# Kernel optimization log

Hardware: AMD Instinct MI355X
Metric: run time of the kernel (lower is better)

Reference implementation:

```python
import jax, jax.numpy as jnp
import numpy as np

N = 20000          # num_node
E = 160000         # num edges (avg degree 8)
IN_N = 64          # in_features_node
IN_E = 32          # in_features_edge
HN = 64            # nhid_node
HE = 64            # nhid_edge
KAPPA = 0.9
ITERS = 8          # fixed Picard iterations for the equilibrium solve


def setup_inputs() -> dict:
    key = jax.random.key(0)
    ks = jax.random.split(key, 16)
    f32 = jnp.float32

    def w(k, shape, fan_in):
        return (jax.random.normal(k, shape, dtype=f32) / np.sqrt(fan_in)).astype(f32)

    return {
        # graph structure (int constants)
        "R": jax.random.randint(ks[0], (E,), 0, N),   # receiver node per edge
        "S": jax.random.randint(ks[1], (E,), 0, N),   # sender node per edge
        "H": jax.random.randint(ks[2], (E,), 0, N),   # edge->node aggregation index
        # features (features-first layout, as in the torch code)
        "node_data": jax.random.normal(ks[3], (IN_N, N), dtype=f32),
        "Ra_data": jax.random.normal(ks[4], (IN_E, E), dtype=f32),
        # INECN_Layer parameters
        "W_es": w(ks[5], (HE, HN), HN),      # sender-message weight
        "W_er": w(ks[6], (HE, HN), HN),      # receiver-message weight
        "Omega_e": w(ks[7], (HE, IN_E), IN_E),
        "Wn": w(ks[8], (HN, HN), HN),        # implicit node-state weight
        "Bm": w(ks[9], (HN, HE), HE),        # edge->node mixing
        "Omega_n": w(ks[10], (HN, IN_N), IN_N),
        # dense head (V_0: nhid->nhid, V_1: nhid->in_features_node)
        "V0_w": w(ks[11], (HN, HN), HN),
        "V0_b": jnp.zeros((HN,), dtype=f32),
        "V1_w": w(ks[12], (IN_N, HN), HN),
        "V1_b": jnp.zeros((IN_N,), dtype=f32),
    }


def reference(R, S, H, node_data, Ra_data, W_es, W_er, Omega_e, Wn, Bm,
              Omega_n, V0_w, V0_b, V1_w, V1_b):
    # spectral-norm style contraction: ||kappa * Wn / ||Wn|||| <= kappa (adj_rho = 1)
    Wn_hat = (KAPPA * Wn) / jnp.maximum(jnp.linalg.norm(Wn), 1.0)

    bias_e = Omega_e @ Ra_data        # [HE, E] injected edge features
    bias_n = Omega_n @ node_data      # [HN, N] injected node features

    def step(X, _):
        # edge update: messages from sender/receiver node states
        He_logits = W_es @ X[:, S] + W_er @ X[:, R] + bias_e      # [HE, E]
        He = jax.nn.relu(He_logits)
        # aggregate edge states back to nodes
        agg = jax.ops.segment_sum(He.T, H, num_segments=N).T      # [HE, N] -> [HE, N]
        # implicit node update (contraction => convergent fixed point)
        X_new = jax.nn.relu(Wn_hat @ X + Bm @ agg + bias_n)       # [HN, N]
        return X_new, None

    X0 = jnp.zeros((HN, N), dtype=node_data.dtype)
    X, _ = jax.lax.scan(step, X0, None, length=ITERS)

    # final edge states / logits at the (approximate) fixed point
    He_logits3 = W_es @ X[:, S] + W_er @ X[:, R] + bias_e         # [HE, E]
    He = jax.nn.relu(He_logits3)

    # dense head: x = V_1(dropout(relu(V_0(x.T))))  (eval mode: dropout = identity)
    x = X.T                                                        # [N, HN]
    x = jax.nn.relu(x @ V0_w.T + V0_b)                             # [N, HN]
    x = x @ V1_w.T + V1_b                                          # [N, IN_N]
    return (x, He, He_logits3)
```

## Files before the change

### kernel.cpp

```cpp
#include <hip/hip_runtime.h>
#include <math.h>

#define KAPPA 0.9f
#define ST 68
#define TN 32

typedef unsigned short u16;

__device__ __forceinline__ float relu_f(float v) { return fmaxf(v, 0.0f); }
__device__ __forceinline__ float bf_lo(unsigned u) { return __uint_as_float(u << 16); }
__device__ __forceinline__ float bf_hi(unsigned u) { return __uint_as_float(u & 0xFFFF0000u); }
__device__ __forceinline__ u16 f2bf(float x) {
  unsigned u = __float_as_uint(x);
  return (u16)((u + 0x7FFFu + ((u >> 16) & 1u)) >> 16);
}
__device__ __forceinline__ unsigned pack2(float a, float b) {
  return (unsigned)f2bf(a) | ((unsigned)f2bf(b) << 16);
}

__global__ __launch_bounds__(256) void wnhat_kernel(const float* __restrict__ Wn,
                                                    float* __restrict__ Wn_hat) {
  __shared__ float red[4];
  int t = threadIdx.x;
  float v[16];
  float s = 0.f;
#pragma unroll
  for (int j = 0; j < 16; ++j) { v[j] = Wn[t + 256 * j]; s += v[j] * v[j]; }
#pragma unroll
  for (int off = 32; off > 0; off >>= 1) s += __shfl_down(s, off, 64);
  if ((t & 63) == 0) red[t >> 6] = s;
  __syncthreads();
  float norm = sqrtf(red[0] + red[1] + red[2] + red[3]);
  float scale = KAPPA / fmaxf(norm, 1.0f);
#pragma unroll
  for (int j = 0; j < 16; ++j) Wn_hat[t + 256 * j] = v[j] * scale;
}

__global__ __launch_bounds__(256) void bias_n_kernel(const float* __restrict__ node_data,
                                                     const float* __restrict__ Om_n,
                                                     float* __restrict__ bias_n, int N) {
  __shared__ float NdT[64][ST];
  __shared__ float Om[64][ST];
  int t = threadIdx.x;
  int n_base = blockIdx.x * 64;
#pragma unroll
  for (int j = 0; j < 16; ++j) {
    int f = t + 256 * j;
    int r = f >> 6, c = f & 63;
    float val = (n_base + c < N) ? node_data[(size_t)r * N + n_base + c] : 0.f;
    NdT[c][r] = val;
    Om[r][c] = Om_n[f];
  }
  __syncthreads();
  int ni = t & 15, h4 = (t >> 4) * 4;
  float acc[4][4] = {};
#pragma unroll 4
  for (int k = 0; k < 64; k += 4) {
    float4 a[4], w[4];
#pragma unroll
    for (int i = 0; i < 4; ++i) a[i] = *(const float4*)&NdT[ni + 16 * i][k];
#pragma unroll
    for (int j = 0; j < 4; ++j) w[j] = *(const float4*)&Om[h4 + j][k];
#pragma unroll
    for (int i = 0; i < 4; ++i)
#pragma unroll
      for (int j = 0; j < 4; ++j)
        acc[i][j] += a[i].x * w[j].x + a[i].y * w[j].y + a[i].z * w[j].z + a[i].w * w[j].w;
  }
#pragma unroll
  for (int i = 0; i < 4; ++i) {
    int n = n_base + ni + 16 * i;
    if (n < N) {
      float4 o = make_float4(acc[i][0], acc[i][1], acc[i][2], acc[i][3]);
      *(float4*)&bias_n[(size_t)n * 64 + h4] = o;
    }
  }
}

__global__ void hist_kernel(const int* __restrict__ H, int* __restrict__ count, int E) {
  int e = blockIdx.x * 256 + threadIdx.x;
  if (e < E) atomicAdd(&count[H[e]], 1);
}

__global__ __launch_bounds__(256) void scan_kernel(int* count, int* row_off, int* cursor,
                                                   int N, int E) {
  __shared__ int offs[256];
  __shared__ int sums[256];
  int t = threadIdx.x;
  int chunk = (N + 255) / 256;
  int lo = t * chunk, hi = min(lo + chunk, N);
  int s = 0;
  for (int n = lo; n < hi; ++n) s += count[n];
  sums[t] = s;
  __syncthreads();
  if (t == 0) {
    int run = 0;
    for (int i = 0; i < 256; ++i) { offs[i] = run; run += sums[i]; }
  }
  __syncthreads();
  int run = offs[t];
  for (int n = lo; n < hi; ++n) {
    int c = count[n];
    row_off[n] = run;
    cursor[n] = run;
    run += c;
  }
  if (t == 0) row_off[N] = E;
}

__global__ void scatter_kernel(const int* __restrict__ H, const int* __restrict__ S,
                               const int* __restrict__ R, int* cursor,
                               int2* __restrict__ SRs, int* __restrict__ inv_perm, int E) {
  int e = blockIdx.x * 256 + threadIdx.x;
  if (e < E) {
    int h = H[e];
    int pos = atomicAdd(&cursor[h], 1);
    SRs[pos] = make_int2(S[e], R[e]);
    inv_perm[e] = pos;
  }
}

__global__ __launch_bounds__(256) void bias_build_kernel(const float* __restrict__ Ra,
                                                         const float* __restrict__ Om_e,
                                                         const int* __restrict__ inv_perm,
                                                         u16* __restrict__ bias_sb, int E) {
  __shared__ float OmT[64][36];
  __shared__ float RaT[64][36];
  int t = threadIdx.x;
  int e_base = blockIdx.x * 64;
#pragma unroll
  for (int j = 0; j < 8; ++j) {
    int f = t + 256 * j;
    int r = f >> 5, c = f & 31;
    OmT[r][c] = Om_e[f];
  }
#pragma unroll
  for (int j = 0; j < 8; ++j) {
    int f = t + 256 * j;
    int r = f >> 6, c = f & 63;
    int ee = e_base + c;
    RaT[c][r] = (ee < E) ? Ra[(size_t)r * E + ee] : 0.f;
  }
  __syncthreads();
  int ei = t & 15, h4 = (t >> 4) * 4;
  float acc[4][4] = {};
#pragma unroll 4
  for (int jj = 0; jj < 32; jj += 4) {
    float4 ra[4], om[4];
#pragma unroll
    for (int i = 0; i < 4; ++i) ra[i] = *(const float4*)&RaT[ei + 16 * i][jj];
#pragma unroll
    for (int j = 0; j < 4; ++j) om[j] = *(const float4*)&OmT[h4 + j][jj];
#pragma unroll
    for (int i = 0; i < 4; ++i)
#pragma unroll
      for (int j = 0; j < 4; ++j)
        acc[i][j] += ra[i].x * om[j].x + ra[i].y * om[j].y + ra[i].z * om[j].z +
                     ra[i].w * om[j].w;
  }
#pragma unroll
  for (int i = 0; i < 4; ++i) {
    int e = e_base + ei + 16 * i;
    if (e < E) {
      int p = inv_perm[e];
      uint2 o;
      o.x = pack2(acc[i][0], acc[i][1]);
      o.y = pack2(acc[i][2], acc[i][3]);
      *(uint2*)&bias_sb[((size_t)p << 6) + h4] = o;
    }
  }
}

template <int FIRST>
__global__ __launch_bounds__(256) void agg_kernel(
    const u16* __restrict__ MSb_in, const u16* __restrict__ MRb_in,
    const u16* __restrict__ bias_sb, const int2* __restrict__ SRs,
    const int* __restrict__ row_off, float* __restrict__ agg, int N) {
  __shared__ float part[4][8][ST];
  int t = threadIdx.x;
  int nl = t >> 5, sp = (t >> 3) & 3, q8 = t & 7;
  int nd = blockIdx.x * 8 + nl;
  float a[8] = {};
  if (nd < N) {
    int r0 = row_off[nd], r1 = row_off[nd + 1];
    for (int p = r0 + sp; p < r1; p += 8) {
      int p1 = p + 4;
      bool has1 = p1 < r1;
      int pc1 = has1 ? p1 : p;
      uint4 bv0 = *(const uint4*)&bias_sb[((size_t)p << 6) + q8 * 8];
      uint4 bv1 = *(const uint4*)&bias_sb[((size_t)pc1 << 6) + q8 * 8];
      if (FIRST) {
        a[0] += relu_f(bf_lo(bv0.x)); a[1] += relu_f(bf_hi(bv0.x));
        a[2] += relu_f(bf_lo(bv0.y)); a[3] += relu_f(bf_hi(bv0.y));
        a[4] += relu_f(bf_lo(bv0.z)); a[5] += relu_f(bf_hi(bv0.z));
        a[6] += relu_f(bf_lo(bv0.w)); a[7] += relu_f(bf_hi(bv0.w));
        if (has1) {
          a[0] += relu_f(bf_lo(bv1.x)); a[1] += relu_f(bf_hi(bv1.x));
          a[2] += relu_f(bf_lo(bv1.y)); a[3] += relu_f(bf_hi(bv1.y));
          a[4] += relu_f(bf_lo(bv1.z)); a[5] += relu_f(bf_hi(bv1.z));
          a[6] += relu_f(bf_lo(bv1.w)); a[7] += relu_f(bf_hi(bv1.w));
        }
      } else {
        int2 sr0 = SRs[p];
        int2 sr1 = SRs[pc1];
        uint4 mv0 = *(const uint4*)&MSb_in[((size_t)sr0.x << 6) + q8 * 8];
        uint4 rv0 = *(const uint4*)&MRb_in[((size_t)sr0.y << 6) + q8 * 8];
        uint4 mv1 = *(const uint4*)&MSb_in[((size_t)sr1.x << 6) + q8 * 8];
        uint4 rv1 = *(const uint4*)&MRb_in[((size_t)sr1.y << 6) + q8 * 8];
        a[0] += relu_f(bf_lo(mv0.x) + bf_lo(rv0.x) + bf_lo(bv0.x));
        a[1] += relu_f(bf_hi(mv0.x) + bf_hi(rv0.x) + bf_hi(bv0.x));
        a[2] += relu_f(bf_lo(mv0.y) + bf_lo(rv0.y) + bf_lo(bv0.y));
        a[3] += relu_f(bf_hi(mv0.y) + bf_hi(rv0.y) + bf_hi(bv0.y));
        a[4] += relu_f(bf_lo(mv0.z) + bf_lo(rv0.z) + bf_lo(bv0.z));
        a[5] += relu_f(bf_hi(mv0.z) + bf_hi(rv0.z) + bf_hi(bv0.z));
        a[6] += relu_f(bf_lo(mv0.w) + bf_lo(rv0.w) + bf_lo(bv0.w));
        a[7] += relu_f(bf_hi(mv0.w) + bf_hi(rv0.w) + bf_hi(bv0.w));
        if (has1) {
          a[0] += relu_f(bf_lo(mv1.x) + bf_lo(rv1.x) + bf_lo(bv1.x));
          a[1] += relu_f(bf_hi(mv1.x) + bf_hi(rv1.x) + bf_hi(bv1.x));
          a[2] += relu_f(bf_lo(mv1.y) + bf_lo(rv1.y) + bf_lo(bv1.y));
          a[3] += relu_f(bf_hi(mv1.y) + bf_hi(rv1.y) + bf_hi(bv1.y));
          a[4] += relu_f(bf_lo(mv1.z) + bf_lo(rv1.z) + bf_lo(bv1.z));
          a[5] += relu_f(bf_hi(mv1.z) + bf_hi(rv1.z) + bf_hi(bv1.z));
          a[6] += relu_f(bf_lo(mv1.w) + bf_lo(rv1.w) + bf_lo(bv1.w));
          a[7] += relu_f(bf_hi(mv1.w) + bf_hi(rv1.w) + bf_hi(bv1.w));
        }
      }
    }
  }
  *(float4*)&part[sp][nl][q8 * 8] = make_float4(a[0], a[1], a[2], a[3]);
  *(float4*)&part[sp][nl][q8 * 8 + 4] = make_float4(a[4], a[5], a[6], a[7]);
  __syncthreads();
  if (sp == 0 && nd < N) {
#pragma unroll
    for (int u = 0; u < 2; ++u) {
      float4 s0 = *(const float4*)&part[0][nl][q8 * 8 + 4 * u];
      float4 s1 = *(const float4*)&part[1][nl][q8 * 8 + 4 * u];
      float4 s2 = *(const float4*)&part[2][nl][q8 * 8 + 4 * u];
      float4 s3 = *(const float4*)&part[3][nl][q8 * 8 + 4 * u];
      float4 o = make_float4(s0.x + s1.x + s2.x + s3.x, s0.y + s1.y + s2.y + s3.y,
                             s0.z + s1.z + s2.z + s3.z, s0.w + s1.w + s2.w + s3.w);
      *(float4*)&agg[(size_t)nd * 64 + q8 * 8 + 4 * u] = o;
    }
  }
}

template <int FIRST, int LAST>
__global__ __launch_bounds__(256) void node_kernel(
    const float* __restrict__ X, const float* __restrict__ agg,
    const float* __restrict__ bias_n, const float* __restrict__ Wn_hat,
    const float* __restrict__ Bm, const float* __restrict__ W_es,
    const float* __restrict__ W_er, const float* __restrict__ V0_w,
    const float* __restrict__ V0_b, const float* __restrict__ V1_w,
    const float* __restrict__ V1_b, float* __restrict__ Xout,
    u16* __restrict__ MSb_out, u16* __restrict__ MRb_out,
    float* __restrict__ head_out, int N) {
  __shared__ float Wa[64][ST], Wb[64][ST];
  __shared__ float Xsh[TN][ST], Ash[TN][ST];
  __shared__ float b0s[64], b1s[64];
  int t = threadIdx.x;
  int n_base = blockIdx.x * TN;
#pragma unroll
  for (int j = 0; j < 16; ++j) {
    int f = t + 256 * j;
    int r = f >> 6, c = f & 63;
    Wa[r][c] = Wn_hat[f];
    Wb[r][c] = Bm[f];
  }
  int n8 = t >> 3;
  int q8 = t & 7;
  int nd = n_base + n8;
  bool ok = nd < N;
  if (!FIRST) {
    float4 x0 = make_float4(0, 0, 0, 0), x1 = x0;
    if (ok) {
      x0 = *(const float4*)&X[(size_t)nd * 64 + q8 * 8];
      x1 = *(const float4*)&X[(size_t)nd * 64 + q8 * 8 + 4];
    }
    *(float4*)&Xsh[n8][q8 * 8] = x0;
    *(float4*)&Xsh[n8][q8 * 8 + 4] = x1;
  }
  {
    float4 a0 = make_float4(0, 0, 0, 0), a1 = a0;
    if (ok) {
      a0 = *(const float4*)&agg[(size_t)nd * 64 + q8 * 8];
      a1 = *(const float4*)&agg[(size_t)nd * 64 + q8 * 8 + 4];
    }
    *(float4*)&Ash[n8][q8 * 8] = a0;
    *(float4*)&Ash[n8][q8 * 8 + 4] = a1;
  }
  __syncthreads();
  int ni = t & 15, h4 = (t >> 4) * 4;
  float acc[2][4] = {};
#pragma unroll 4
  for (int k = 0; k < 64; k += 4) {
    float4 xv[2], av[2], wv[4], bv[4];
#pragma unroll
    for (int i = 0; i < 2; ++i) {
      if (!FIRST) xv[i] = *(const float4*)&Xsh[ni + 16 * i][k];
      av[i] = *(const float4*)&Ash[ni + 16 * i][k];
    }
#pragma unroll
    for (int j = 0; j < 4; ++j) {
      wv[j] = *(const float4*)&Wa[h4 + j][k];
      bv[j] = *(const float4*)&Wb[h4 + j][k];
    }
#pragma unroll
    for (int i = 0; i < 2; ++i)
#pragma unroll
      for (int j = 0; j < 4; ++j) {
        float v = av[i].x * bv[j].x + av[i].y * bv[j].y + av[i].z * bv[j].z +
                  av[i].w * bv[j].w;
        if (!FIRST)
          v += xv[i].x * wv[j].x + xv[i].y * wv[j].y + xv[i].z * wv[j].z +
               xv[i].w * wv[j].w;
        acc[i][j] += v;
      }
  }
  __syncthreads();
#pragma unroll
  for (int i = 0; i < 2; ++i) {
    int nn = n_base + ni + 16 * i;
    float4 bb = make_float4(0, 0, 0, 0);
    if (nn < N) bb = *(const float4*)&bias_n[(size_t)nn * 64 + h4];
    float x0 = relu_f(acc[i][0] + bb.x);
    float x1 = relu_f(acc[i][1] + bb.y);
    float x2 = relu_f(acc[i][2] + bb.z);
    float x3 = relu_f(acc[i][3] + bb.w);
    if (!LAST && nn < N)
      *(float4*)&Xout[(size_t)nn * 64 + h4] = make_float4(x0, x1, x2, x3);
    *(float4*)&Xsh[ni + 16 * i][h4] = make_float4(x0, x1, x2, x3);
  }
#pragma unroll
  for (int j = 0; j < 16; ++j) {
    int f = t + 256 * j;
    int r = f >> 6, c = f & 63;
    Wa[r][c] = W_es[f];
    Wb[r][c] = W_er[f];
  }
  __syncthreads();
  {
    float ma[2][4] = {}, ra[2][4] = {};
#pragma unroll 4
    for (int k = 0; k < 64; k += 4) {
      float4 xv[2], ws[4], wr[4];
#pragma unroll
      for (int i = 0; i < 2; ++i) xv[i] = *(const float4*)&Xsh[ni + 16 * i][k];
#pragma unroll
      for (int j = 0; j < 4; ++j) {
        ws[j] = *(const float4*)&Wa[h4 + j][k];
        wr[j] = *(const float4*)&Wb[h4 + j][k];
      }
#pragma unroll
      for (int i = 0; i < 2; ++i)
#pragma unroll
        for (int j = 0; j < 4; ++j) {
          ma[i][j] += xv[i].x * ws[j].x + xv[i].y * ws[j].y + xv[i].z * ws[j].z +
                      xv[i].w * ws[j].w;
          ra[i][j] += xv[i].x * wr[j].x + xv[i].y * wr[j].y + xv[i].z * wr[j].z +
                      xv[i].w * wr[j].w;
        }
    }
#pragma unroll
    for (int i = 0; i < 2; ++i) {
      int nn = n_base + ni + 16 * i;
      if (nn < N) {
        uint2 om, orr;
        om.x = pack2(ma[i][0], ma[i][1]);
        om.y = pack2(ma[i][2], ma[i][3]);
        orr.x = pack2(ra[i][0], ra[i][1]);
        orr.y = pack2(ra[i][2], ra[i][3]);
        *(uint2*)&MSb_out[((size_t)nn << 6) + h4] = om;
        *(uint2*)&MRb_out[((size_t)nn << 6) + h4] = orr;
      }
    }
  }
  if (LAST) {
    __syncthreads();
#pragma unroll
    for (int j = 0; j < 16; ++j) {
      int f = t + 256 * j;
      int r = f >> 6, c = f & 63;
      Wa[r][c] = V0_w[f];
      Wb[r][c] = V1_w[f];
    }
    if (t < 64) b0s[t] = V0_b[t];
    else if (t < 128) b1s[t - 64] = V1_b[t - 64];
    __syncthreads();
    float c1[2][4] = {};
#pragma unroll 4
    for (int k = 0; k < 64; k += 4) {
      float4 xv[2], wv[4];
#pragma unroll
      for (int i = 0; i < 2; ++i) xv[i] = *(const float4*)&Xsh[ni + 16 * i][k];
#pragma unroll
      for (int j = 0; j < 4; ++j) wv[j] = *(const float4*)&Wa[h4 + j][k];
#pragma unroll
      for (int i = 0; i < 2; ++i)
#pragma unroll
        for (int j = 0; j < 4; ++j)
          c1[i][j] += xv[i].x * wv[j].x + xv[i].y * wv[j].y + xv[i].z * wv[j].z +
                      xv[i].w * wv[j].w;
    }
    __syncthreads();
#pragma unroll
    for (int i = 0; i < 2; ++i) {
      float4 o;
      o.x = relu_f(c1[i][0] + b0s[h4 + 0]);
      o.y = relu_f(c1[i][1] + b0s[h4 + 1]);
      o.z = relu_f(c1[i][2] + b0s[h4 + 2]);
      o.w = relu_f(c1[i][3] + b0s[h4 + 3]);
      *(float4*)&Xsh[ni + 16 * i][h4] = o;
    }
    __syncthreads();
    float c2[2][4] = {};
#pragma unroll 4
    for (int k = 0; k < 64; k += 4) {
      float4 xv[2], wv[4];
#pragma unroll
      for (int i = 0; i < 2; ++i) xv[i] = *(const float4*)&Xsh[ni + 16 * i][k];
#pragma unroll
      for (int j = 0; j < 4; ++j) wv[j] = *(const float4*)&Wb[h4 + j][k];
#pragma unroll
      for (int i = 0; i < 2; ++i)
#pragma unroll
        for (int j = 0; j < 4; ++j)
          c2[i][j] += xv[i].x * wv[j].x + xv[i].y * wv[j].y + xv[i].z * wv[j].z +
                      xv[i].w * wv[j].w;
    }
#pragma unroll
    for (int i = 0; i < 2; ++i) {
      int nn = n_base + ni + 16 * i;
      if (nn < N) {
        float4 o;
        o.x = c2[i][0] + b1s[h4 + 0];
        o.y = c2[i][1] + b1s[h4 + 1];
        o.z = c2[i][2] + b1s[h4 + 2];
        o.w = c2[i][3] + b1s[h4 + 3];
        *(float4*)&head_out[(size_t)nn * 64 + h4] = o;
      }
    }
  }
}

__global__ __launch_bounds__(256) void edge_final_kernel(
    const u16* __restrict__ MSb, const u16* __restrict__ MRb,
    const int* __restrict__ S, const int* __restrict__ R,
    const float* __restrict__ Om_e, const float* __restrict__ Ra,
    float* __restrict__ He_out, float* __restrict__ Hel_out, int E) {
  __shared__ float T[64][ST];
  __shared__ float pool2[4608];
  int t = threadIdx.x;
  int e_base = blockIdx.x * 64;
#pragma unroll
  for (int j = 0; j < 8; ++j) {
    int f = t + 256 * j;
    int r = f >> 5, c = f & 31;
    pool2[r * 36 + c] = Om_e[f];
  }
#pragma unroll
  for (int j = 0; j < 8; ++j) {
    int f = t + 256 * j;
    int r = f >> 6, c = f & 63;
    int e2 = e_base + c;
    pool2[2304 + c * 36 + r] = (e2 < E) ? Ra[(size_t)r * E + e2] : 0.f;
  }
  {
    int e = t >> 2, q = t & 3;
    int ee = e_base + e;
    int ec = (ee < E) ? ee : 0;
    int s = S[ec], r = R[ec];
    const u16* mp = &MSb[((size_t)s << 6) + q * 16];
    const u16* rp = &MRb[((size_t)r << 6) + q * 16];
    uint4 m0 = *(const uint4*)mp;
    uint4 m1 = *(const uint4*)(mp + 8);
    uint4 r0 = *(const uint4*)rp;
    uint4 r1 = *(const uint4*)(rp + 8);
    float* tp = &T[e][q * 16];
    tp[0] = bf_lo(m0.x) + bf_lo(r0.x);
    tp[1] = bf_hi(m0.x) + bf_hi(r0.x);
    tp[2] = bf_lo(m0.y) + bf_lo(r0.y);
    tp[3] = bf_hi(m0.y) + bf_hi(r0.y);
    tp[4] = bf_lo(m0.z) + bf_lo(r0.z);
    tp[5] = bf_hi(m0.z) + bf_hi(r0.z);
    tp[6] = bf_lo(m0.w) + bf_lo(r0.w);
    tp[7] = bf_hi(m0.w) + bf_hi(r0.w);
    tp[8] = bf_lo(m1.x) + bf_lo(r1.x);
    tp[9] = bf_hi(m1.x) + bf_hi(r1.x);
    tp[10] = bf_lo(m1.y) + bf_lo(r1.y);
    tp[11] = bf_hi(m1.y) + bf_hi(r1.y);
    tp[12] = bf_lo(m1.z) + bf_lo(r1.z);
    tp[13] = bf_hi(m1.z) + bf_hi(r1.z);
    tp[14] = bf_lo(m1.w) + bf_lo(r1.w);
    tp[15] = bf_hi(m1.w) + bf_hi(r1.w);
  }
  __syncthreads();
  int ei = t & 15, h4 = (t >> 4) * 4;
  float acc[4][4] = {};
#pragma unroll 4
  for (int jj = 0; jj < 32; jj += 4) {
    float4 ra[4], om[4];
#pragma unroll
    for (int i = 0; i < 4; ++i)
      ra[i] = *(const float4*)&pool2[2304 + (ei + 16 * i) * 36 + jj];
#pragma unroll
    for (int j = 0; j < 4; ++j) om[j] = *(const float4*)&pool2[(h4 + j) * 36 + jj];
#pragma unroll
    for (int i = 0; i < 4; ++i)
#pragma unroll
      for (int j = 0; j < 4; ++j)
        acc[i][j] += ra[i].x * om[j].x + ra[i].y * om[j].y + ra[i].z * om[j].z +
                     ra[i].w * om[j].w;
  }
#pragma unroll
  for (int i = 0; i < 4; ++i) {
    float4 tv = *(const float4*)&T[ei + 16 * i][h4];
    acc[i][0] += tv.x;
    acc[i][1] += tv.y;
    acc[i][2] += tv.z;
    acc[i][3] += tv.w;
  }
  __syncthreads();
#pragma unroll
  for (int i = 0; i < 4; ++i)
#pragma unroll
    for (int j = 0; j < 4; ++j)
      pool2[(ei + 16 * i) * 65 + h4 + j] = acc[i][j];
  __syncthreads();
  {
    int e4 = (t & 15) * 4, h0 = t >> 4;
#pragma unroll
    for (int rep = 0; rep < 4; ++rep) {
      int h = h0 + 16 * rep;
      float4 v;
      v.x = pool2[(e4 + 0) * 65 + h];
      v.y = pool2[(e4 + 1) * 65 + h];
      v.z = pool2[(e4 + 2) * 65 + h];
      v.w = pool2[(e4 + 3) * 65 + h];
      size_t idx = (size_t)h * E + e_base + e4;
      if (e_base + e4 < E) {
        *(float4*)&Hel_out[idx] = v;
        float4 u = make_float4(relu_f(v.x), relu_f(v.y), relu_f(v.z), relu_f(v.w));
        *(float4*)&He_out[idx] = u;
      }
    }
  }
}

extern "C" void kernel_launch(void* const* d_in, const int* in_sizes, int n_in,
                              void* d_out, int out_size, void* d_ws, size_t ws_size,
                              hipStream_t stream) {
  const int* R = (const int*)d_in[0];
  const int* S = (const int*)d_in[1];
  const int* H = (const int*)d_in[2];
  const float* node_data = (const float*)d_in[3];
  const float* Ra = (const float*)d_in[4];
  const float* W_es = (const float*)d_in[5];
  const float* W_er = (const float*)d_in[6];
  const float* Om_e = (const float*)d_in[7];
  const float* Wn = (const float*)d_in[8];
  const float* Bm = (const float*)d_in[9];
  const float* Om_n = (const float*)d_in[10];
  const float* V0_w = (const float*)d_in[11];
  const float* V0_b = (const float*)d_in[12];
  const float* V1_w = (const float*)d_in[13];
  const float* V1_b = (const float*)d_in[14];
  const int E = in_sizes[0];
  const int N = in_sizes[3] / 64;
  const size_t N64 = (size_t)N * 64;

  float* ws = (float*)d_ws;
  float* Wn_hat = ws;
  float* bias_n = Wn_hat + 4096;
  float* X0 = bias_n + N64;
  float* X1p = X0 + N64;
  u16* MSb_B = (u16*)(X1p + N64);
  u16* MRb_B = MSb_B + N64;
  int* row_off = (int*)(MRb_B + N64);
  int* cursor = row_off + (N + 1);
  int2* SRs = (int2*)(cursor + N);
  int* inv_perm = (int*)(SRs + E);

  float* out = (float*)d_out;
  float* out_x = out;
  float* out_He = out + N64;
  float* out_Hel = out_He + (size_t)64 * E;
  u16* bias_sb = (u16*)out_He;
  u16* MSb_A = (u16*)out_Hel;
  u16* MRb_A = MSb_A + N64;
  float* aggf = (float*)(MRb_A + N64);

  int nb_node = (N + 63) / 64;
  int nb_iter = (N + TN - 1) / TN;
  int nb_agg = (N + 7) / 8;
  int nb_edge = (E + 63) / 64;
  int nb_flat = (E + 255) / 256;

  hipMemsetAsync(cursor, 0, (size_t)N * sizeof(int), stream);
  wnhat_kernel<<<1, 256, 0, stream>>>(Wn, Wn_hat);
  bias_n_kernel<<<nb_node, 256, 0, stream>>>(node_data, Om_n, bias_n, N);
  hist_kernel<<<nb_flat, 256, 0, stream>>>(H, cursor, E);
  scan_kernel<<<1, 256, 0, stream>>>(cursor, row_off, cursor, N, E);
  scatter_kernel<<<nb_flat, 256, 0, stream>>>(H, S, R, cursor, SRs, inv_perm, E);
  bias_build_kernel<<<nb_edge, 256, 0, stream>>>(Ra, Om_e, inv_perm, bias_sb, E);

  float* Xa = X0;
  float* Xb = X1p;
  const u16* msi = nullptr;
  const u16* mri = nullptr;
  for (int it = 0; it < 8; ++it) {
    u16* mso = (it & 1) ? MSb_B : MSb_A;
    u16* mro = (it & 1) ? MRb_B : MRb_A;
    if (it == 0) {
      agg_kernel<1><<<nb_agg, 256, 0, stream>>>(nullptr, nullptr, bias_sb, SRs,
                                                row_off, aggf, N);
      node_kernel<1, 0><<<nb_iter, 256, 0, stream>>>(
          Xa, aggf, bias_n, Wn_hat, Bm, W_es, W_er, V0_w, V0_b, V1_w, V1_b,
          Xb, mso, mro, out_x, N);
    } else if (it < 7) {
      agg_kernel<0><<<nb_agg, 256, 0, stream>>>(msi, mri, bias_sb, SRs,
                                                row_off, aggf, N);
      node_kernel<0, 0><<<nb_iter, 256, 0, stream>>>(
          Xa, aggf, bias_n, Wn_hat, Bm, W_es, W_er, V0_w, V0_b, V1_w, V1_b,
          Xb, mso, mro, out_x, N);
    } else {
      agg_kernel<0><<<nb_agg, 256, 0, stream>>>(msi, mri, bias_sb, SRs,
                                                row_off, aggf, N);
      node_kernel<0, 1><<<nb_iter, 256, 0, stream>>>(
          Xa, aggf, bias_n, Wn_hat, Bm, W_es, W_er, V0_w, V0_b, V1_w, V1_b,
          Xb, mso, mro, out_x, N);
    }
    msi = mso;
    mri = mro;
    float* tmp = Xa; Xa = Xb; Xb = tmp;
  }
  edge_final_kernel<<<nb_edge, 256, 0, stream>>>(MSb_B, MRb_B, S, R, Om_e, Ra,
                                                 out_He, out_Hel, E);
}
```

Before: 431.5 us.

## Split edge/node message buffers into feature halves and aggregate per half

Bias, message and aggregate buffers change from a [row][64] layout to two planes of [row][32], one per 32-feature half. Aggregation runs as two launches, one per half, so each launch's gathered working set (message tables for N nodes) is half as large and more likely to stay in cache. Bias loads become nontemporal. The node and final-edge kernels are updated to read and write the new layout. The cost is twice as many aggregation launches, each re-reading the CSR indices and row offsets.

```diff
diff --git a/kernel.cpp b/kernel.cpp
--- a/kernel.cpp
+++ b/kernel.cpp
@@ -6,6 +6,7 @@
 #define TN 32
 
 typedef unsigned short u16;
+typedef unsigned uv4 __attribute__((ext_vector_type(4)));
 
 __device__ __forceinline__ float relu_f(float v) { return fmaxf(v, 0.0f); }
 __device__ __forceinline__ float bf_lo(unsigned u) { return __uint_as_float(u << 16); }
@@ -16,6 +17,10 @@
 }
 __device__ __forceinline__ unsigned pack2(float a, float b) {
   return (unsigned)f2bf(a) | ((unsigned)f2bf(b) << 16);
+}
+__device__ __forceinline__ uint4 nt_load_u4(const u16* p) {
+  uv4 v = __builtin_nontemporal_load((const uv4*)p);
+  return make_uint4(v.x, v.y, v.z, v.w);
 }
 
 __global__ __launch_bounds__(256) void wnhat_kernel(const float* __restrict__ Wn,
@@ -123,7 +128,8 @@
 __global__ __launch_bounds__(256) void bias_build_kernel(const float* __restrict__ Ra,
                                                          const float* __restrict__ Om_e,
                                                          const int* __restrict__ inv_perm,
-                                                         u16* __restrict__ bias_sb, int E) {
+                                                         u16* __restrict__ bias_sb,
+                                                         int E) {
   __shared__ float OmT[64][36];
   __shared__ float RaT[64][36];
   int t = threadIdx.x;
@@ -166,20 +172,20 @@
       uint2 o;
       o.x = pack2(acc[i][0], acc[i][1]);
       o.y = pack2(acc[i][2], acc[i][3]);
-      *(uint2*)&bias_sb[((size_t)p << 6) + h4] = o;
+      *(uint2*)&bias_sb[((size_t)(h4 >> 5) * E + p) * 32 + (h4 & 31)] = o;
     }
   }
 }
 
 template <int FIRST>
 __global__ __launch_bounds__(256) void agg_kernel(
-    const u16* __restrict__ MSb_in, const u16* __restrict__ MRb_in,
-    const u16* __restrict__ bias_sb, const int2* __restrict__ SRs,
-    const int* __restrict__ row_off, float* __restrict__ agg, int N) {
-  __shared__ float part[4][8][ST];
+    const u16* __restrict__ MSh, const u16* __restrict__ MRh,
+    const u16* __restrict__ biash, const int2* __restrict__ SRs,
+    const int* __restrict__ row_off, float* __restrict__ aggh, int N) {
+  __shared__ float part[4][16][36];
   int t = threadIdx.x;
-  int nl = t >> 5, sp = (t >> 3) & 3, q8 = t & 7;
-  int nd = blockIdx.x * 8 + nl;
+  int q4 = t & 3, sp = (t >> 2) & 3, nl = t >> 4;
+  int nd = blockIdx.x * 16 + nl;
   float a[8] = {};
   if (nd < N) {
     int r0 = row_off[nd], r1 = row_off[nd + 1];
@@ -187,8 +193,8 @@
       int p1 = p + 4;
       bool has1 = p1 < r1;
       int pc1 = has1 ? p1 : p;
-      uint4 bv0 = *(const uint4*)&bias_sb[((size_t)p << 6) + q8 * 8];
-      uint4 bv1 = *(const uint4*)&bias_sb[((size_t)pc1 << 6) + q8 * 8];
+      uint4 bv0 = nt_load_u4(&biash[((size_t)p << 5) + q4 * 8]);
+      uint4 bv1 = nt_load_u4(&biash[((size_t)pc1 << 5) + q4 * 8]);
       if (FIRST) {
         a[0] += relu_f(bf_lo(bv0.x)); a[1] += relu_f(bf_hi(bv0.x));
         a[2] += relu_f(bf_lo(bv0.y)); a[3] += relu_f(bf_hi(bv0.y));
@@ -203,10 +209,10 @@
       } else {
         int2 sr0 = SRs[p];
         int2 sr1 = SRs[pc1];
-        uint4 mv0 = *(const uint4*)&MSb_in[((size_t)sr0.x << 6) + q8 * 8];
-        uint4 rv0 = *(const uint4*)&MRb_in[((size_t)sr0.y << 6) + q8 * 8];
-        uint4 mv1 = *(const uint4*)&MSb_in[((size_t)sr1.x << 6) + q8 * 8];
-        uint4 rv1 = *(const uint4*)&MRb_in[((size_t)sr1.y << 6) + q8 * 8];
+        uint4 mv0 = *(const uint4*)&MSh[((size_t)sr0.x << 5) + q4 * 8];
+        uint4 rv0 = *(const uint4*)&MRh[((size_t)sr0.y << 5) + q4 * 8];
+        uint4 mv1 = *(const uint4*)&MSh[((size_t)sr1.x << 5) + q4 * 8];
+        uint4 rv1 = *(const uint4*)&MRh[((size_t)sr1.y << 5) + q4 * 8];
         a[0] += relu_f(bf_lo(mv0.x) + bf_lo(rv0.x) + bf_lo(bv0.x));
         a[1] += relu_f(bf_hi(mv0.x) + bf_hi(rv0.x) + bf_hi(bv0.x));
         a[2] += relu_f(bf_lo(mv0.y) + bf_lo(rv0.y) + bf_lo(bv0.y));
@@ -228,19 +234,19 @@
       }
     }
   }
-  *(float4*)&part[sp][nl][q8 * 8] = make_float4(a[0], a[1], a[2], a[3]);
-  *(float4*)&part[sp][nl][q8 * 8 + 4] = make_float4(a[4], a[5], a[6], a[7]);
+  *(float4*)&part[sp][nl][q4 * 8] = make_float4(a[0], a[1], a[2], a[3]);
+  *(float4*)&part[sp][nl][q4 * 8 + 4] = make_float4(a[4], a[5], a[6], a[7]);
   __syncthreads();
   if (sp == 0 && nd < N) {
 #pragma unroll
     for (int u = 0; u < 2; ++u) {
-      float4 s0 = *(const float4*)&part[0][nl][q8 * 8 + 4 * u];
-      float4 s1 = *(const float4*)&part[1][nl][q8 * 8 + 4 * u];
-      float4 s2 = *(const float4*)&part[2][nl][q8 * 8 + 4 * u];
-      float4 s3 = *(const float4*)&part[3][nl][q8 * 8 + 4 * u];
+      float4 s0 = *(const float4*)&part[0][nl][q4 * 8 + 4 * u];
+      float4 s1 = *(const float4*)&part[1][nl][q4 * 8 + 4 * u];
+      float4 s2 = *(const float4*)&part[2][nl][q4 * 8 + 4 * u];
+      float4 s3 = *(const float4*)&part[3][nl][q4 * 8 + 4 * u];
       float4 o = make_float4(s0.x + s1.x + s2.x + s3.x, s0.y + s1.y + s2.y + s3.y,
                              s0.z + s1.z + s2.z + s3.z, s0.w + s1.w + s2.w + s3.w);
-      *(float4*)&agg[(size_t)nd * 64 + q8 * 8 + 4 * u] = o;
+      *(float4*)&aggh[(size_t)nd * 32 + q4 * 8 + 4 * u] = o;
     }
   }
 }
@@ -283,8 +289,9 @@
   {
     float4 a0 = make_float4(0, 0, 0, 0), a1 = a0;
     if (ok) {
-      a0 = *(const float4*)&agg[(size_t)nd * 64 + q8 * 8];
-      a1 = *(const float4*)&agg[(size_t)nd * 64 + q8 * 8 + 4];
+      const float* ap = &agg[((size_t)(q8 >> 2) * N + nd) * 32 + (q8 & 3) * 8];
+      a0 = *(const float4*)ap;
+      a1 = *(const float4*)(ap + 4);
     }
     *(float4*)&Ash[n8][q8 * 8] = a0;
     *(float4*)&Ash[n8][q8 * 8 + 4] = a1;
@@ -370,8 +377,9 @@
         om.y = pack2(ma[i][2], ma[i][3]);
         orr.x = pack2(ra[i][0], ra[i][1]);
         orr.y = pack2(ra[i][2], ra[i][3]);
-        *(uint2*)&MSb_out[((size_t)nn << 6) + h4] = om;
-        *(uint2*)&MRb_out[((size_t)nn << 6) + h4] = orr;
+        size_t base = ((size_t)(h4 >> 5) * N + nn) * 32 + (h4 & 31);
+        *(uint2*)&MSb_out[base] = om;
+        *(uint2*)&MRb_out[base] = orr;
       }
     }
   }
@@ -447,7 +455,7 @@
     const u16* __restrict__ MSb, const u16* __restrict__ MRb,
     const int* __restrict__ S, const int* __restrict__ R,
     const float* __restrict__ Om_e, const float* __restrict__ Ra,
-    float* __restrict__ He_out, float* __restrict__ Hel_out, int E) {
+    float* __restrict__ He_out, float* __restrict__ Hel_out, int E, int N) {
   __shared__ float T[64][ST];
   __shared__ float pool2[4608];
   int t = threadIdx.x;
@@ -470,8 +478,9 @@
     int ee = e_base + e;
     int ec = (ee < E) ? ee : 0;
     int s = S[ec], r = R[ec];
-    const u16* mp = &MSb[((size_t)s << 6) + q * 16];
-    const u16* rp = &MRb[((size_t)r << 6) + q * 16];
+    size_t boff = ((size_t)(q >> 1) * N) * 32 + (q & 1) * 16;
+    const u16* mp = &MSb[boff + (size_t)s * 32];
+    const u16* rp = &MRb[boff + (size_t)r * 32];
     uint4 m0 = *(const uint4*)mp;
     uint4 m1 = *(const uint4*)(mp + 8);
     uint4 r0 = *(const uint4*)rp;
@@ -568,6 +577,8 @@
   const int E = in_sizes[0];
   const int N = in_sizes[3] / 64;
   const size_t N64 = (size_t)N * 64;
+  const size_t N32 = (size_t)N * 32;
+  const size_t E32 = (size_t)E * 32;
 
   float* ws = (float*)d_ws;
   float* Wn_hat = ws;
@@ -592,7 +603,7 @@
 
   int nb_node = (N + 63) / 64;
   int nb_iter = (N + TN - 1) / TN;
-  int nb_agg = (N + 7) / 8;
+  int nb_agg = (N + 15) / 16;
   int nb_edge = (E + 63) / 64;
   int nb_flat = (E + 255) / 256;
 
@@ -612,20 +623,26 @@
     u16* mso = (it & 1) ? MSb_B : MSb_A;
     u16* mro = (it & 1) ? MRb_B : MRb_A;
     if (it == 0) {
-      agg_kernel<1><<<nb_agg, 256, 0, stream>>>(nullptr, nullptr, bias_sb, SRs,
-                                                row_off, aggf, N);
+      for (int hf = 0; hf < 2; ++hf)
+        agg_kernel<1><<<nb_agg, 256, 0, stream>>>(nullptr, nullptr,
+                                                  bias_sb + hf * E32, SRs, row_off,
+                                                  aggf + hf * N32, N);
       node_kernel<1, 0><<<nb_iter, 256, 0, stream>>>(
           Xa, aggf, bias_n, Wn_hat, Bm, W_es, W_er, V0_w, V0_b, V1_w, V1_b,
           Xb, mso, mro, out_x, N);
     } else if (it < 7) {
-      agg_kernel<0><<<nb_agg, 256, 0, stream>>>(msi, mri, bias_sb, SRs,
-                                                row_off, aggf, N);
+      for (int hf = 0; hf < 2; ++hf)
+        agg_kernel<0><<<nb_agg, 256, 0, stream>>>(msi + hf * N32, mri + hf * N32,
+                                                  bias_sb + hf * E32, SRs, row_off,
+                                                  aggf + hf * N32, N);
       node_kernel<0, 0><<<nb_iter, 256, 0, stream>>>(
           Xa, aggf, bias_n, Wn_hat, Bm, W_es, W_er, V0_w, V0_b, V1_w, V1_b,
           Xb, mso, mro, out_x, N);
     } else {
-      agg_kernel<0><<<nb_agg, 256, 0, stream>>>(msi, mri, bias_sb, SRs,
-                                                row_off, aggf, N);
+      for (int hf = 0; hf < 2; ++hf)
+        agg_kernel<0><<<nb_agg, 256, 0, stream>>>(msi + hf * N32, mri + hf * N32,
+                                                  bias_sb + hf * E32, SRs, row_off,
+                                                  aggf + hf * N32, N);
       node_kernel<0, 1><<<nb_iter, 256, 0, stream>>>(
           Xa, aggf, bias_n, Wn_hat, Bm, W_es, W_er, V0_w, V0_b, V1_w, V1_b,
           Xb, mso, mro, out_x, N);
@@ -635,5 +652,5 @@
     float* tmp = Xa; Xa = Xb; Xb = tmp;
   }
   edge_final_kernel<<<nb_edge, 256, 0, stream>>>(MSb_B, MRb_B, S, R, Om_e, Ra,
-                                                 out_He, out_Hel, E);
-}
+                                                 out_He, out_Hel, E, N);
+}
```

After: 472.0 us. 9.4% more time.
